# Kernel tuning notes

Measured on AMD Instinct MI355X. Metric: run time of the kernel, lower is better.

Reference implementation:

```python
import jax, jax.numpy as jnp
import numpy as np

B, N, K, C, D_IN, D_OUT = 64, 207, 32, 8, 64, 64


def setup_inputs() -> dict:
    key = jax.random.key(0)
    k1, k2, k3 = jax.random.split(key, 3)
    clustered_index_topk = jax.random.randint(k1, (B, N, K), 0, C)
    weightedDinput_topk = jax.random.normal(k2, (B, N, K, D_IN), dtype=jnp.float32)
    W = jax.random.normal(k3, (C, D_OUT, D_IN), dtype=jnp.float32) * 0.05
    return {"clustered_index_topk": clustered_index_topk,
            "weightedDinput_topk": weightedDinput_topk,
            "W": W}


def reference(clustered_index_topk, weightedDinput_topk, W):
    # one-hot over classes: [B, N, K, C]
    onehot = (clustered_index_topk[..., None] == jnp.arange(C)).astype(weightedDinput_topk.dtype)
    # per-class masked sum over top-k neighbors: [B, N, C, D_IN]
    sums = jnp.einsum('bnkc,bnkd->bncd', onehot, weightedDinput_topk)
    # per-class counts, clamped to >= 1 (matches torch.clamp(class_count, 1))
    counts = jnp.maximum(onehot.sum(axis=2), 1.0)  # [B, N, C]
    mean = sums / counts[..., None]
    # per-class Linear (weight [out, in], no bias) + Tanh -> [B, N, C, D_OUT]
    out = jnp.tanh(jnp.einsum('bncd,cod->bnco', mean, W))
    return out
```

## Files before the change

kernel.cpp:

```cpp
#include <hip/hip_runtime.h>
#include <cstddef>

#define BB 64
#define NN 207
#define KK 32
#define CC 8
#define DIN 64
#define DOUT 64
#define TILE 8
#define PAIR 16
#define NP 13
#define MPAD 68

typedef float vfloat4 __attribute__((ext_vector_type(4)));

__device__ __forceinline__ float fast_tanh(float v) {
    float e = __expf(2.0f * v);
    return 1.0f - 2.0f * __builtin_amdgcn_rcpf(e + 1.0f);
}

__device__ __forceinline__ void nt_store4(float* p, float a, float b, float c, float d) {
    vfloat4 r; r.x = a; r.y = b; r.z = c; r.w = d;
    __builtin_nontemporal_store(r, (vfloat4*)p);
}

__device__ __forceinline__ void fma16(float4& a, const float4 m,
                                      const float4 w0, const float4 w1,
                                      const float4 w2, const float4 w3) {
    a.x = fmaf(m.x, w0.x, a.x); a.y = fmaf(m.x, w0.y, a.y);
    a.z = fmaf(m.x, w0.z, a.z); a.w = fmaf(m.x, w0.w, a.w);
    a.x = fmaf(m.y, w1.x, a.x); a.y = fmaf(m.y, w1.y, a.y);
    a.z = fmaf(m.y, w1.z, a.z); a.w = fmaf(m.y, w1.w, a.w);
    a.x = fmaf(m.z, w2.x, a.x); a.y = fmaf(m.z, w2.y, a.y);
    a.z = fmaf(m.z, w2.z, a.z); a.w = fmaf(m.z, w2.w, a.w);
    a.x = fmaf(m.w, w3.x, a.x); a.y = fmaf(m.w, w3.y, a.y);
    a.z = fmaf(m.w, w3.z, a.z); a.w = fmaf(m.w, w3.w, a.w);
}

template<bool USE_WT>
__device__ __forceinline__ void load_w4(const float* __restrict__ Wtc,
                                        const float* __restrict__ Wc,
                                        int o0, int dc,
                                        float4& w0, float4& w1, float4& w2, float4& w3) {
    if (USE_WT) {
        w0 = *(const float4*)(Wtc + (size_t)(dc * 4 + 0) * DOUT);
        w1 = *(const float4*)(Wtc + (size_t)(dc * 4 + 1) * DOUT);
        w2 = *(const float4*)(Wtc + (size_t)(dc * 4 + 2) * DOUT);
        w3 = *(const float4*)(Wtc + (size_t)(dc * 4 + 3) * DOUT);
    } else {
        float4 a0 = *(const float4*)(Wc + (size_t)(o0 + 0) * DIN + dc * 4);
        float4 a1 = *(const float4*)(Wc + (size_t)(o0 + 1) * DIN + dc * 4);
        float4 a2 = *(const float4*)(Wc + (size_t)(o0 + 2) * DIN + dc * 4);
        float4 a3 = *(const float4*)(Wc + (size_t)(o0 + 3) * DIN + dc * 4);
        w0 = make_float4(a0.x, a1.x, a2.x, a3.x);
        w1 = make_float4(a0.y, a1.y, a2.y, a3.y);
        w2 = make_float4(a0.z, a1.z, a2.z, a3.z);
        w3 = make_float4(a0.w, a1.w, a2.w, a3.w);
    }
}

__global__ __launch_bounds__(256) void transpose_W_kernel(
    const float* __restrict__ W, float* __restrict__ Wt)
{
    __shared__ float t[DIN * (DOUT + 1)];
    const int c   = blockIdx.x;
    const int tid = threadIdx.x;
    const float* __restrict__ Wc  = W  + (size_t)c * DOUT * DIN;
    float* __restrict__       Wtc = Wt + (size_t)c * DIN * DOUT;
    #pragma unroll
    for (int r = 0; r < 16; ++r) {
        const int i = r * 256 + tid;
        const int o = i >> 6, d = i & 63;
        t[d * (DOUT + 1) + o] = Wc[i];
    }
    __syncthreads();
    #pragma unroll
    for (int r = 0; r < 16; ++r) {
        const int i = r * 256 + tid;
        const int d = i >> 6, o = i & 63;
        Wtc[i] = t[d * (DOUT + 1) + o];
    }
}

template<bool USE_WT>
__global__ __launch_bounds__(256, 4) void ordered_gcn_kernel(
    const int* __restrict__ idx,
    const float* __restrict__ x,
    const float* __restrict__ W,
    const float* __restrict__ Wt,
    float* __restrict__ out)
{
    __shared__ int   idx_s[PAIR * KK];
    __shared__ float inv_s[PAIR * CC];
    __shared__ float meanA[TILE * CC * MPAD];
    __shared__ float meanB[TILE * CC * MPAD];

    const int tid = threadIdx.x;
    const int b   = blockIdx.y;
    const int n0  = blockIdx.x * PAIR;

    #pragma unroll
    for (int r = 0; r < 2; ++r) {
        const int i = r * 256 + tid;
        const int P = i >> 5, k = i & 31;
        int n = n0 + P; if (n > NN - 1) n = NN - 1;
        idx_s[i] = idx[((size_t)(b * NN + n)) * KK + k];
    }
    __syncthreads();

    if (tid < PAIR * CC) {
        const int P = tid >> 3, c = tid & 7;
        int cnt = 0;
        #pragma unroll
        for (int k = 0; k < KK; ++k) cnt += (idx_s[P * KK + k] == c) ? 1 : 0;
        inv_s[tid] = 1.0f / (float)(cnt > 1 ? cnt : 1);
    }

    const int p  = tid >> 5;
    const int d2 = (tid & 31) * 2;
    int na = n0 + p;        if (na > NN - 1) na = NN - 1;
    int nb = n0 + TILE + p; if (nb > NN - 1) nb = NN - 1;
    const float* __restrict__ xp0 = x + ((size_t)(b * NN + na)) * KK * DIN + d2;
    const float* __restrict__ xp1 = x + ((size_t)(b * NN + nb)) * KK * DIN + d2;

    float2 acc0[CC];
    #pragma unroll
    for (int c = 0; c < CC; ++c) acc0[c] = make_float2(0.f, 0.f);
    #pragma unroll 1
    for (int g = 0; g < 4; ++g) {
        float2 v[8];
        #pragma unroll
        for (int j = 0; j < 8; ++j)
            v[j] = *(const float2*)(xp0 + (size_t)(g * 8 + j) * DIN);
        #pragma unroll
        for (int j = 0; j < 8; ++j) {
            const int ca = idx_s[p * KK + g * 8 + j];
            #pragma unroll
            for (int c = 0; c < CC; ++c) {
                const float mf = (ca == c) ? 1.0f : 0.0f;
                acc0[c].x = fmaf(mf, v[j].x, acc0[c].x);
                acc0[c].y = fmaf(mf, v[j].y, acc0[c].y);
            }
        }
    }
    __syncthreads();
    #pragma unroll
    for (int c = 0; c < CC; ++c) {
        const float s = inv_s[p * CC + c];
        float2 m; m.x = acc0[c].x * s; m.y = acc0[c].y * s;
        *(float2*)(&meanA[(p * CC + c) * MPAD + d2]) = m;
    }
    __syncthreads();

    const int ph = tid >> 7;
    const int c2 = (tid >> 4) & 7;
    const int o0 = (tid & 15) * 4;
    const float* __restrict__ Wtc = Wt + (size_t)c2 * DIN * DOUT + o0;
    const float* __restrict__ Wc  = W  + (size_t)c2 * DOUT * DIN;

    float4 acc2[4];
    #pragma unroll
    for (int pp = 0; pp < 4; ++pp) acc2[pp] = make_float4(0.f, 0.f, 0.f, 0.f);
    float2 acc1[CC];
    #pragma unroll
    for (int c = 0; c < CC; ++c) acc1[c] = make_float2(0.f, 0.f);

    #pragma unroll 1
    for (int g = 0; g < 4; ++g) {
        float2 v[8];
        #pragma unroll
        for (int j = 0; j < 8; ++j)
            v[j] = *(const float2*)(xp1 + (size_t)(g * 8 + j) * DIN);

        #pragma unroll
        for (int dq = 0; dq < 4; ++dq) {
            const int dc = g * 4 + dq;
            float4 w0, w1, w2, w3;
            load_w4<USE_WT>(Wtc, Wc, o0, dc, w0, w1, w2, w3);
            #pragma unroll
            for (int pp = 0; pp < 4; ++pp) {
                const float4 m = *(const float4*)(&meanA[((ph * 4 + pp) * CC + c2) * MPAD + dc * 4]);
                fma16(acc2[pp], m, w0, w1, w2, w3);
            }
        }

        #pragma unroll
        for (int j = 0; j < 8; ++j) {
            const int ca = idx_s[(TILE + p) * KK + g * 8 + j];
            #pragma unroll
            for (int c = 0; c < CC; ++c) {
                const float mf = (ca == c) ? 1.0f : 0.0f;
                acc1[c].x = fmaf(mf, v[j].x, acc1[c].x);
                acc1[c].y = fmaf(mf, v[j].y, acc1[c].y);
            }
        }
    }

    #pragma unroll
    for (int c = 0; c < CC; ++c) {
        const float s = inv_s[(TILE + p) * CC + c];
        float2 m; m.x = acc1[c].x * s; m.y = acc1[c].y * s;
        *(float2*)(&meanB[(p * CC + c) * MPAD + d2]) = m;
    }
    __syncthreads();

    #pragma unroll
    for (int pp = 0; pp < 4; ++pp) {
        const int nn = n0 + ph * 4 + pp;
        if (nn < NN) {
            nt_store4(out + (((size_t)(b * NN + nn)) * CC + c2) * DOUT + o0,
                      fast_tanh(acc2[pp].x), fast_tanh(acc2[pp].y),
                      fast_tanh(acc2[pp].z), fast_tanh(acc2[pp].w));
        }
    }

    float4 acc3[4];
    #pragma unroll
    for (int pp = 0; pp < 4; ++pp) acc3[pp] = make_float4(0.f, 0.f, 0.f, 0.f);
    #pragma unroll 1
    for (int dc = 0; dc < 16; ++dc) {
        float4 w0, w1, w2, w3;
        load_w4<USE_WT>(Wtc, Wc, o0, dc, w0, w1, w2, w3);
        #pragma unroll
        for (int pp = 0; pp < 4; ++pp) {
            const float4 m = *(const float4*)(&meanB[((ph * 4 + pp) * CC + c2) * MPAD + dc * 4]);
            fma16(acc3[pp], m, w0, w1, w2, w3);
        }
    }
    #pragma unroll
    for (int pp = 0; pp < 4; ++pp) {
        const int nn = n0 + TILE + ph * 4 + pp;
        if (nn < NN) {
            nt_store4(out + (((size_t)(b * NN + nn)) * CC + c2) * DOUT + o0,
                      fast_tanh(acc3[pp].x), fast_tanh(acc3[pp].y),
                      fast_tanh(acc3[pp].z), fast_tanh(acc3[pp].w));
        }
    }
}

extern "C" void kernel_launch(void* const* d_in, const int* in_sizes, int n_in,
                              void* d_out, int out_size, void* d_ws, size_t ws_size,
                              hipStream_t stream) {
    const int*   idx = (const int*)d_in[0];
    const float* x   = (const float*)d_in[1];
    const float* W   = (const float*)d_in[2];
    float* out = (float*)d_out;
    float* Wt  = (float*)d_ws;

    dim3 grid(NP, BB);
    dim3 block(256);
    const size_t wt_bytes = (size_t)CC * DIN * DOUT * sizeof(float);
    if (ws_size >= wt_bytes) {
        transpose_W_kernel<<<dim3(CC), block, 0, stream>>>(W, Wt);
        ordered_gcn_kernel<true><<<grid, block, 0, stream>>>(idx, x, W, Wt, out);
    } else {
        ordered_gcn_kernel<false><<<grid, block, 0, stream>>>(idx, x, W, Wt, out);
    }
}
```

Measured before the change: 208.6 us.

## Replace two-phase pipelined tile with single-pass 16-node tile using bf16 shared means

Removes the software pipeline that overlapped the second half-tile's aggregation with the first half's matmul. All 16 nodes are now aggregated in one pass using float4 loads per thread, and the per-class means are stored in shared memory as bf16. The matmul stage then runs once over 8 nodes per thread. Occupancy hint rises to 6 blocks per SM and output stores become regular instead of nontemporal. The bf16 means reduce LDS footprint but lose precision, which could exceed tolerance, and dropping the overlap exposes global-load latency.

```diff
diff --git a/kernel.cpp b/kernel.cpp
--- a/kernel.cpp
+++ b/kernel.cpp
@@ -7,21 +7,18 @@
 #define CC 8
 #define DIN 64
 #define DOUT 64
-#define TILE 8
-#define PAIR 16
-#define NP 13
-#define MPAD 68
-
-typedef float vfloat4 __attribute__((ext_vector_type(4)));
+#define TILE 16
+#define NT 13
+#define MPADH 68
 
 __device__ __forceinline__ float fast_tanh(float v) {
     float e = __expf(2.0f * v);
     return 1.0f - 2.0f * __builtin_amdgcn_rcpf(e + 1.0f);
 }
 
-__device__ __forceinline__ void nt_store4(float* p, float a, float b, float c, float d) {
-    vfloat4 r; r.x = a; r.y = b; r.z = c; r.w = d;
-    __builtin_nontemporal_store(r, (vfloat4*)p);
+__device__ __forceinline__ unsigned int f2bf(float f) {
+    union { float f; unsigned int u; } v; v.f = f;
+    return (v.u + 0x7fffu + ((v.u >> 16) & 1u)) >> 16;
 }
 
 __device__ __forceinline__ void fma16(float4& a, const float4 m,
@@ -83,21 +80,20 @@
 }
 
 template<bool USE_WT>
-__global__ __launch_bounds__(256, 4) void ordered_gcn_kernel(
+__global__ __launch_bounds__(256, 6) void ordered_gcn_kernel(
     const int* __restrict__ idx,
     const float* __restrict__ x,
     const float* __restrict__ W,
     const float* __restrict__ Wt,
     float* __restrict__ out)
 {
-    __shared__ int   idx_s[PAIR * KK];
-    __shared__ float inv_s[PAIR * CC];
-    __shared__ float meanA[TILE * CC * MPAD];
-    __shared__ float meanB[TILE * CC * MPAD];
+    __shared__ int            idx_s[TILE * KK];
+    __shared__ float          inv_s[TILE * CC];
+    __shared__ unsigned short mean_s[TILE * CC * MPADH];
 
     const int tid = threadIdx.x;
     const int b   = blockIdx.y;
-    const int n0  = blockIdx.x * PAIR;
+    const int n0  = blockIdx.x * TILE;
 
     #pragma unroll
     for (int r = 0; r < 2; ++r) {
@@ -108,7 +104,7 @@
     }
     __syncthreads();
 
-    if (tid < PAIR * CC) {
+    if (tid < TILE * CC) {
         const int P = tid >> 3, c = tid & 7;
         int cnt = 0;
         #pragma unroll
@@ -116,124 +112,104 @@
         inv_s[tid] = 1.0f / (float)(cnt > 1 ? cnt : 1);
     }
 
-    const int p  = tid >> 5;
-    const int d2 = (tid & 31) * 2;
-    int na = n0 + p;        if (na > NN - 1) na = NN - 1;
-    int nb = n0 + TILE + p; if (nb > NN - 1) nb = NN - 1;
-    const float* __restrict__ xp0 = x + ((size_t)(b * NN + na)) * KK * DIN + d2;
-    const float* __restrict__ xp1 = x + ((size_t)(b * NN + nb)) * KK * DIN + d2;
-
-    float2 acc0[CC];
-    #pragma unroll
-    for (int c = 0; c < CC; ++c) acc0[c] = make_float2(0.f, 0.f);
-    #pragma unroll 1
-    for (int g = 0; g < 4; ++g) {
-        float2 v[8];
-        #pragma unroll
-        for (int j = 0; j < 8; ++j)
-            v[j] = *(const float2*)(xp0 + (size_t)(g * 8 + j) * DIN);
-        #pragma unroll
-        for (int j = 0; j < 8; ++j) {
-            const int ca = idx_s[p * KK + g * 8 + j];
-            #pragma unroll
-            for (int c = 0; c < CC; ++c) {
-                const float mf = (ca == c) ? 1.0f : 0.0f;
-                acc0[c].x = fmaf(mf, v[j].x, acc0[c].x);
-                acc0[c].y = fmaf(mf, v[j].y, acc0[c].y);
-            }
+    {
+        const int p  = tid >> 4;
+        const int d4 = (tid & 15) * 4;
+        int n = n0 + p; if (n > NN - 1) n = NN - 1;
+        const float* __restrict__ xp = x + ((size_t)(b * NN + n)) * KK * DIN + d4;
+
+        float4 acc[CC];
+        #pragma unroll
+        for (int c = 0; c < CC; ++c) acc[c] = make_float4(0.f, 0.f, 0.f, 0.f);
+
+        #pragma unroll 1
+        for (int g = 0; g < 2; ++g) {
+            float4 v[8];
+            #pragma unroll
+            for (int j = 0; j < 8; ++j)
+                v[j] = *(const float4*)(xp + (size_t)(g * 8 + j) * DIN);
+            #pragma unroll
+            for (int j = 0; j < 8; ++j) {
+                const int ca = idx_s[p * KK + g * 8 + j];
+                #pragma unroll
+                for (int c = 0; c < CC; ++c) {
+                    const float mf = (ca == c) ? 1.0f : 0.0f;
+                    acc[c].x = fmaf(mf, v[j].x, acc[c].x);
+                    acc[c].y = fmaf(mf, v[j].y, acc[c].y);
+                    acc[c].z = fmaf(mf, v[j].z, acc[c].z);
+                    acc[c].w = fmaf(mf, v[j].w, acc[c].w);
+                }
+            }
+        }
+        #pragma unroll 1
+        for (int g = 2; g < 4; ++g) {
+            float4 v[8];
+            #pragma unroll
+            for (int j = 0; j < 8; ++j)
+                v[j] = *(const float4*)(xp + (size_t)(g * 8 + j) * DIN);
+            #pragma unroll
+            for (int j = 0; j < 8; ++j) {
+                const int ca = idx_s[p * KK + g * 8 + j];
+                #pragma unroll
+                for (int c = 0; c < CC; ++c) {
+                    const float mf = (ca == c) ? 1.0f : 0.0f;
+                    acc[c].x = fmaf(mf, v[j].x, acc[c].x);
+                    acc[c].y = fmaf(mf, v[j].y, acc[c].y);
+                    acc[c].z = fmaf(mf, v[j].z, acc[c].z);
+                    acc[c].w = fmaf(mf, v[j].w, acc[c].w);
+                }
+            }
+        }
+        __syncthreads();
+
+        #pragma unroll
+        for (int c = 0; c < CC; ++c) {
+            const float s = inv_s[p * CC + c];
+            const unsigned int lo = f2bf(acc[c].x * s) | (f2bf(acc[c].y * s) << 16);
+            const unsigned int hi = f2bf(acc[c].z * s) | (f2bf(acc[c].w * s) << 16);
+            *(uint2*)(&mean_s[(p * CC + c) * MPADH + d4]) = make_uint2(lo, hi);
         }
     }
     __syncthreads();
-    #pragma unroll
-    for (int c = 0; c < CC; ++c) {
-        const float s = inv_s[p * CC + c];
-        float2 m; m.x = acc0[c].x * s; m.y = acc0[c].y * s;
-        *(float2*)(&meanA[(p * CC + c) * MPAD + d2]) = m;
-    }
-    __syncthreads();
-
-    const int ph = tid >> 7;
-    const int c2 = (tid >> 4) & 7;
-    const int o0 = (tid & 15) * 4;
-    const float* __restrict__ Wtc = Wt + (size_t)c2 * DIN * DOUT + o0;
-    const float* __restrict__ Wc  = W  + (size_t)c2 * DOUT * DIN;
-
-    float4 acc2[4];
-    #pragma unroll
-    for (int pp = 0; pp < 4; ++pp) acc2[pp] = make_float4(0.f, 0.f, 0.f, 0.f);
-    float2 acc1[CC];
-    #pragma unroll
-    for (int c = 0; c < CC; ++c) acc1[c] = make_float2(0.f, 0.f);
-
-    #pragma unroll 1
-    for (int g = 0; g < 4; ++g) {
-        float2 v[8];
-        #pragma unroll
-        for (int j = 0; j < 8; ++j)
-            v[j] = *(const float2*)(xp1 + (size_t)(g * 8 + j) * DIN);
-
-        #pragma unroll
-        for (int dq = 0; dq < 4; ++dq) {
-            const int dc = g * 4 + dq;
+
+    {
+        const int ph = tid >> 7;
+        const int c2 = (tid >> 4) & 7;
+        const int o0 = (tid & 15) * 4;
+        const float* __restrict__ Wtc = Wt + (size_t)c2 * DIN * DOUT + o0;
+        const float* __restrict__ Wc  = W  + (size_t)c2 * DOUT * DIN;
+
+        float4 acc2[8];
+        #pragma unroll
+        for (int pp = 0; pp < 8; ++pp) acc2[pp] = make_float4(0.f, 0.f, 0.f, 0.f);
+
+        #pragma unroll 2
+        for (int dc = 0; dc < 16; ++dc) {
             float4 w0, w1, w2, w3;
             load_w4<USE_WT>(Wtc, Wc, o0, dc, w0, w1, w2, w3);
             #pragma unroll
-            for (int pp = 0; pp < 4; ++pp) {
-                const float4 m = *(const float4*)(&meanA[((ph * 4 + pp) * CC + c2) * MPAD + dc * 4]);
+            for (int pp = 0; pp < 8; ++pp) {
+                const uint2 mw = *(const uint2*)(&mean_s[((ph * 8 + pp) * CC + c2) * MPADH + dc * 4]);
+                float4 m;
+                m.x = __uint_as_float(mw.x << 16);
+                m.y = __uint_as_float(mw.x & 0xffff0000u);
+                m.z = __uint_as_float(mw.y << 16);
+                m.w = __uint_as_float(mw.y & 0xffff0000u);
                 fma16(acc2[pp], m, w0, w1, w2, w3);
             }
         }
 
         #pragma unroll
-        for (int j = 0; j < 8; ++j) {
-            const int ca = idx_s[(TILE + p) * KK + g * 8 + j];
-            #pragma unroll
-            for (int c = 0; c < CC; ++c) {
-                const float mf = (ca == c) ? 1.0f : 0.0f;
-                acc1[c].x = fmaf(mf, v[j].x, acc1[c].x);
-                acc1[c].y = fmaf(mf, v[j].y, acc1[c].y);
-            }
-        }
-    }
-
-    #pragma unroll
-    for (int c = 0; c < CC; ++c) {
-        const float s = inv_s[(TILE + p) * CC + c];
-        float2 m; m.x = acc1[c].x * s; m.y = acc1[c].y * s;
-        *(float2*)(&meanB[(p * CC + c) * MPAD + d2]) = m;
-    }
-    __syncthreads();
-
-    #pragma unroll
-    for (int pp = 0; pp < 4; ++pp) {
-        const int nn = n0 + ph * 4 + pp;
-        if (nn < NN) {
-            nt_store4(out + (((size_t)(b * NN + nn)) * CC + c2) * DOUT + o0,
-                      fast_tanh(acc2[pp].x), fast_tanh(acc2[pp].y),
-                      fast_tanh(acc2[pp].z), fast_tanh(acc2[pp].w));
-        }
-    }
-
-    float4 acc3[4];
-    #pragma unroll
-    for (int pp = 0; pp < 4; ++pp) acc3[pp] = make_float4(0.f, 0.f, 0.f, 0.f);
-    #pragma unroll 1
-    for (int dc = 0; dc < 16; ++dc) {
-        float4 w0, w1, w2, w3;
-        load_w4<USE_WT>(Wtc, Wc, o0, dc, w0, w1, w2, w3);
-        #pragma unroll
-        for (int pp = 0; pp < 4; ++pp) {
-            const float4 m = *(const float4*)(&meanB[((ph * 4 + pp) * CC + c2) * MPAD + dc * 4]);
-            fma16(acc3[pp], m, w0, w1, w2, w3);
-        }
-    }
-    #pragma unroll
-    for (int pp = 0; pp < 4; ++pp) {
-        const int nn = n0 + TILE + ph * 4 + pp;
-        if (nn < NN) {
-            nt_store4(out + (((size_t)(b * NN + nn)) * CC + c2) * DOUT + o0,
-                      fast_tanh(acc3[pp].x), fast_tanh(acc3[pp].y),
-                      fast_tanh(acc3[pp].z), fast_tanh(acc3[pp].w));
+        for (int pp = 0; pp < 8; ++pp) {
+            const int nn = n0 + ph * 8 + pp;
+            if (nn < NN) {
+                float4 r;
+                r.x = fast_tanh(acc2[pp].x);
+                r.y = fast_tanh(acc2[pp].y);
+                r.z = fast_tanh(acc2[pp].z);
+                r.w = fast_tanh(acc2[pp].w);
+                *(float4*)(out + (((size_t)(b * NN + nn)) * CC + c2) * DOUT + o0) = r;
+            }
         }
     }
 }
@@ -247,7 +223,7 @@
     float* out = (float*)d_out;
     float* Wt  = (float*)d_ws;
 
-    dim3 grid(NP, BB);
+    dim3 grid(NT, BB);
     dim3 block(256);
     const size_t wt_bytes = (size_t)CC * DIN * DOUT * sizeof(float);
     if (ws_size >= wt_bytes) {
```

Measured after the change: 205.4 us. Within noise of the previous version (-1.6%).
